# Kernel optimization log

Measured on AMD Instinct MI355X. Metric: run time of the kernel, lower is better.

Reference implementation:

```python
import jax, jax.numpy as jnp
import numpy as np

N_NODES = 100000
N_EDGES = 3200000
IN_CH = 256
HIDDEN = 64
OUT_CH = 128


def setup_inputs() -> dict:
    key = jax.random.key(0)
    ks = jax.random.split(key, 6)
    x = jax.random.normal(ks[0], (N_NODES, IN_CH), dtype=jnp.float32)
    edge_index = jax.random.randint(ks[1], (2, N_EDGES), 0, N_NODES, dtype=jnp.int64)
    W1 = jax.random.normal(ks[2], (IN_CH, HIDDEN), dtype=jnp.float32) * (1.0 / np.sqrt(IN_CH))
    b1 = jnp.zeros((HIDDEN,), dtype=jnp.float32)
    W2 = jax.random.normal(ks[3], (HIDDEN, OUT_CH), dtype=jnp.float32) * (1.0 / np.sqrt(HIDDEN))
    b2 = jnp.zeros((OUT_CH,), dtype=jnp.float32)
    fcW = jax.random.normal(ks[4], (2, OUT_CH), dtype=jnp.float32) * (1.0 / np.sqrt(OUT_CH))
    fcb = jnp.zeros((2,), dtype=jnp.float32)
    return {"x": x, "edge_index": edge_index, "W1": W1, "b1": b1,
            "W2": W2, "b2": b2, "fcW": fcW, "fcb": fcb}


def _gcn_conv(x, edge_index, W, b):
    """PyG GCNConv: linear transform, add self-loops, symmetric D^-1/2 A D^-1/2 aggregation, bias."""
    N = x.shape[0]
    h = x @ W  # [N, F_out]
    loops = jnp.arange(N, dtype=edge_index.dtype)
    row = jnp.concatenate([edge_index[0], loops])  # source nodes
    col = jnp.concatenate([edge_index[1], loops])  # destination nodes
    deg = jax.ops.segment_sum(jnp.ones_like(col, dtype=h.dtype), col, num_segments=N)
    dinv = jnp.where(deg > 0, jax.lax.rsqrt(deg), 0.0)
    norm = dinv[row] * dinv[col]  # [E+N]
    out = jax.ops.segment_sum(h[row] * norm[:, None], col, num_segments=N)
    return out + b


def reference(x, edge_index, W1, b1, W2, b2, fcW, fcb):
    h = jax.nn.relu(_gcn_conv(x, edge_index, W1, b1))
    h = jax.nn.relu(_gcn_conv(h, edge_index, W2, b2))
    g = jnp.mean(h, axis=0)  # [OUT_CH]
    return g @ fcW.T + fcb   # [2]
```

## Files before the change

kernel.cpp:

```cpp
#include <hip/hip_runtime.h>

#define N_NODES 100000
#define N_EDGES 3200000
#define C_IN 256
#define C_H 64
#define C_OUT 128
#define NB 391
#define BCAP 16384
#define G2F 625
#define NTILES 6250
#define NT16 6250
#define G_GM 1563
#define CH1 8192

typedef unsigned int u32;
typedef unsigned short u16;
typedef unsigned char u8;
typedef unsigned long long u64;
typedef __attribute__((ext_vector_type(8))) short bf16x8;
typedef __attribute__((ext_vector_type(4))) float f32x4;

typedef __attribute__((address_space(3))) unsigned int l_u32;
typedef __attribute__((address_space(1))) const unsigned int g_u32;

__device__ __forceinline__ float bf2f(u16 u) {
    union { u32 i; float f; } v; v.i = ((u32)u) << 16; return v.f;
}
__device__ __forceinline__ u16 f2bf(float f) {
    union { float f; u32 i; } v; v.f = f;
    u32 x = v.i;
    return (u16)((x + 0x7fffu + ((x >> 16) & 1u)) >> 16);
}
__device__ __forceinline__ u8 f2fp8(float f) {
    union { float f; u32 i; } v; v.f = f;
    u32 s = (v.i >> 24) & 0x80u;
    float a = __builtin_fabsf(f);
    a = fminf(a, 448.f);
    if (a < 0.015625f) {
        int m = (int)__builtin_rintf(a * 512.f);
        return (u8)(s | (u32)m);
    }
    union { float ff; u32 i; } w; w.ff = a;
    u32 x = w.i;
    u32 r = x + 0x7FFFFu + ((x >> 20) & 1u);
    u32 E = (r >> 23) - 120u;
    u32 m = (r >> 20) & 7u;
    return (u8)(s | (E << 3) | m);
}

__device__ __forceinline__ void gll16(const void* gp, const void* lp) {
    __builtin_amdgcn_global_load_lds((g_u32*)gp, (l_u32*)lp, 16, 0, 0);
}

__global__ __launch_bounds__(256) void k_prep(const void* __restrict__ x, const void* __restrict__ ei,
                                              const void* __restrict__ W1, const void* __restrict__ W2,
                                              const void* __restrict__ b1, const void* __restrict__ b2,
                                              const void* __restrict__ fcW, const void* __restrict__ fcb,
                                              int* __restrict__ flags,
                                              u16* __restrict__ W1m, u16* __restrict__ W2m,
                                              u32* __restrict__ bucket_cnt,
                                              float* __restrict__ b1c, float* __restrict__ b2c,
                                              float* __restrict__ fcWc, float* __restrict__ fcbc) {
    __shared__ int sfb;
    int b = blockIdx.x, t = threadIdx.x;
    if (t < 64) {
        u32 wv = ((const u32*)x)[t];
        u32 low = wv & 0xffffu;
        int e = (int)((low >> 7) & 0xff);
        bool inw = (e > 96 && e < 160) || (low == 0);
        u64 m = __ballot(inw);
        if (t == 0) sfb = (__popcll(m) >= 60) ? 1 : 0;
    } else if (b == 0 && t < 128) {
        int i = t - 64;
        u32 wv = ((const u32*)ei)[2 * i + 1];
        u64 m = __ballot(wv == 0);
        if (i == 0) flags[1] = (m == ~0ull) ? 1 : 0;
    }
    __syncthreads();
    int isbf = sfb;
    if (b == 0 && t == 0) flags[0] = isbf;
    int i = b * 256 + t;
    if (i < NB) bucket_cnt[i] = 0;
    if (i < C_IN * C_H) {
        const u16* w1b = (const u16*)W1; const float* w1f = (const float*)W1;
        int j = i & 7, lane = (i >> 3) & 63, nt = (i >> 9) & 3, k0 = i >> 11;
        int k = k0 * 32 + ((lane >> 4) & 3) * 8 + j;
        int n = nt * 16 + (lane & 15);
        W1m[i] = isbf ? w1b[k * C_H + n] : f2bf(w1f[k * C_H + n]);
    } else {
        int i2 = i - C_IN * C_H;
        const u16* w2b = (const u16*)W2; const float* w2f = (const float*)W2;
        int j = i2 & 7, lane = (i2 >> 3) & 63, nt = (i2 >> 9) & 7, k0 = (i2 >> 12) & 1;
        int k = k0 * 32 + ((lane >> 4) & 3) * 8 + j;
        int n = nt * 16 + (lane & 15);
        W2m[i2] = isbf ? w2b[k * C_OUT + n] : f2bf(w2f[k * C_OUT + n]);
    }
    if (b == 0) {
        if (isbf) {
            const u16* p1 = (const u16*)b1;  const u16* p2 = (const u16*)b2;
            const u16* pw = (const u16*)fcW; const u16* pb = (const u16*)fcb;
            for (int q = t; q < C_H; q += 256) b1c[q] = bf2f(p1[q]);
            for (int q = t; q < C_OUT; q += 256) b2c[q] = bf2f(p2[q]);
            for (int q = t; q < 2 * C_OUT; q += 256) fcWc[q] = bf2f(pw[q]);
            for (int q = t; q < 2; q += 256) fcbc[q] = bf2f(pb[q]);
        } else {
            const float* p1 = (const float*)b1;  const float* p2 = (const float*)b2;
            const float* pw = (const float*)fcW; const float* pb = (const float*)fcb;
            for (int q = t; q < C_H; q += 256) b1c[q] = p1[q];
            for (int q = t; q < C_OUT; q += 256) b2c[q] = p2[q];
            for (int q = t; q < 2 * C_OUT; q += 256) fcWc[q] = pw[q];
            for (int q = t; q < 2; q += 256) fcbc[q] = pb[q];
        }
    }
}

__global__ __launch_bounds__(512) void k_scatter1(const int* __restrict__ ei,
                                                  const int* __restrict__ flags,
                                                  u32* __restrict__ bucket_cnt,
                                                  u32* __restrict__ ebuf) {
    __shared__ u32 cnt[NB];
    __shared__ u32 lcur[NB];
    __shared__ u32 gbase[NB];
    __shared__ u32 lofs[512];
    __shared__ u32 stp[CH1];
    __shared__ u16 stb[CH1];
    int t = threadIdx.x;
    int is64 = flags[1];
    int e0 = blockIdx.x * CH1;
    int nv = min(CH1, N_EDGES - e0);
    for (int i = t; i < NB; i += 512) { cnt[i] = 0; lcur[i] = 0; }
    __syncthreads();
    for (int i = t; i < nv; i += 512) {
        int e = e0 + i;
        int d = is64 ? ei[2 * (N_EDGES + e)] : ei[N_EDGES + e];
        atomicAdd(&cnt[d >> 8], 1u);
    }
    __syncthreads();
    u32 v = (t < NB) ? cnt[t] : 0;
    lofs[t] = v;
    __syncthreads();
    for (int off = 1; off < 512; off <<= 1) {
        u32 a = (t >= off) ? lofs[t - off] : 0;
        __syncthreads();
        lofs[t] += a;
        __syncthreads();
    }
    u32 excl = lofs[t] - v;
    __syncthreads();
    lofs[t] = excl;
    __syncthreads();
    for (int i = t; i < nv; i += 512) {
        int e = e0 + i;
        int d, s;
        if (is64) { d = ei[2 * (N_EDGES + e)]; s = ei[2 * e]; }
        else      { d = ei[N_EDGES + e];       s = ei[e]; }
        int b = d >> 8;
        u32 slot = lofs[b] + atomicAdd(&lcur[b], 1u);
        stp[slot] = ((u32)(d & 255) << 20) | (u32)s;
        stb[slot] = (u16)b;
    }
    __syncthreads();
    for (int b = t; b < NB; b += 512) {
        u32 c = cnt[b];
        gbase[b] = c ? atomicAdd(&bucket_cnt[b], c) : 0;
    }
    __syncthreads();
    for (int s = t; s < nv; s += 512) {
        int b = stb[s];
        ebuf[(size_t)b * BCAP + gbase[b] + (s - lofs[b])] = stp[s];
    }
}

__global__ __launch_bounds__(256) void k_scatter2(const u32* __restrict__ bucket_cnt,
                                                  const u32* __restrict__ ebuf,
                                                  int* __restrict__ rowptr,
                                                  float* __restrict__ dinv,
                                                  int* __restrict__ csr) {
    __shared__ u32 ssum[256];
    __shared__ u32 snev;
    __shared__ int cnt[256];
    __shared__ int pfx[256];
    __shared__ int lcur[256];
    int b = blockIdx.x, t = threadIdx.x;
    u32 a = 0;
    for (int i = t; i < NB; i += 256) {
        u32 cv = bucket_cnt[i];
        if (i < b) a += cv;
        if (i == b) snev = cv;
    }
    ssum[t] = a;
    __syncthreads();
    for (int off = 128; off >= 1; off >>= 1) {
        if (t < off) ssum[t] += ssum[t + off];
        __syncthreads();
    }
    int ebeg = (int)ssum[0];
    int ne = (int)snev;
    const u32* src = ebuf + (size_t)b * BCAP;
    int sbeg = ebeg + (b << 8);
    cnt[t] = 0;
    lcur[t] = 0;
    __syncthreads();
    for (int i = t; i < ne; i += 256)
        atomicAdd(&cnt[(src[i] >> 20) & 255], 1);
    __syncthreads();
    int v = cnt[t];
    pfx[t] = v;
    __syncthreads();
    for (int off = 1; off < 256; off <<= 1) {
        int pv = (t >= off) ? pfx[t - off] : 0;
        __syncthreads();
        pfx[t] += pv;
        __syncthreads();
    }
    int node = (b << 8) + t;
    int rstart = sbeg + (pfx[t] - v) + t;
    if (node < N_NODES) {
        rowptr[node] = rstart;
        dinv[node] = rsqrtf((float)(v + 1));
        csr[rstart] = node << 6;
        if (node == N_NODES - 1) {
            rowptr[N_NODES] = rstart + v + 1;
            for (int i = 0; i < 64; ++i) csr[rstart + v + 1 + i] = 0;
        }
    }
    __syncthreads();
    for (int i = t; i < ne; i += 256) {
        u32 p = src[i];
        int dl = (p >> 20) & 255;
        int pos = sbeg + (pfx[dl] - cnt[dl]) + dl + 1 + atomicAdd(&lcur[dl], 1);
        csr[pos] = (int)((p & 0x1FFFFu) << 6);
    }
}

__global__ __launch_bounds__(256) void k_gemm1(const void* __restrict__ xv,
                                               const u16* __restrict__ W1m,
                                               const float* __restrict__ dinv,
                                               u8* __restrict__ g1,
                                               const int* __restrict__ flags) {
    __shared__ u16 wlds[C_IN * C_H];
    int t = threadIdx.x;
    int isbf = flags[0];
    {
        const uint4* src = (const uint4*)W1m;
        uint4* dst = (uint4*)wlds;
#pragma unroll
        for (int it = 0; it < 8; ++it) dst[t + it * 256] = src[t + it * 256];
    }
    __syncthreads();
    int w = t >> 6, lane = t & 63;
    int quad = lane >> 4, mrow = lane & 15;
    int m0 = blockIdx.x * 128 + w * 32;
    if (m0 >= N_NODES) return;

    bf16x8 a[2][8];
    if (isbf) {
        const u16* xb = (const u16*)xv;
#pragma unroll
        for (int mt = 0; mt < 2; ++mt)
#pragma unroll
            for (int k0 = 0; k0 < 8; ++k0)
                a[mt][k0] = *(const bf16x8*)(xb + (size_t)(m0 + mt * 16 + mrow) * C_IN + k0 * 32 + quad * 8);
    } else {
        const float* xf = (const float*)xv;
#pragma unroll
        for (int mt = 0; mt < 2; ++mt)
#pragma unroll
            for (int k0 = 0; k0 < 8; ++k0) {
                const float* p = xf + (size_t)(m0 + mt * 16 + mrow) * C_IN + k0 * 32 + quad * 8;
                float4 v0 = *(const float4*)p;
                float4 v1 = *(const float4*)(p + 4);
                bf16x8 r;
                r[0] = (short)f2bf(v0.x); r[1] = (short)f2bf(v0.y);
                r[2] = (short)f2bf(v0.z); r[3] = (short)f2bf(v0.w);
                r[4] = (short)f2bf(v1.x); r[5] = (short)f2bf(v1.y);
                r[6] = (short)f2bf(v1.z); r[7] = (short)f2bf(v1.w);
                a[mt][k0] = r;
            }
    }

    float dv0[4], dv1[4];
#pragma unroll
    for (int r = 0; r < 4; ++r) {
        dv0[r] = dinv[m0 + quad * 4 + r] * 16.f;
        dv1[r] = dinv[m0 + 16 + quad * 4 + r] * 16.f;
    }

#pragma unroll
    for (int nt = 0; nt < 4; ++nt) {
        bf16x8 b[8];
#pragma unroll
        for (int k0 = 0; k0 < 8; ++k0)
            b[k0] = *(const bf16x8*)&wlds[((k0 * 4 + nt) * 64 + lane) * 8];
        f32x4 acc0 = {0.f, 0.f, 0.f, 0.f};
        f32x4 acc1 = {0.f, 0.f, 0.f, 0.f};
#pragma unroll
        for (int k0 = 0; k0 < 8; ++k0) {
            acc0 = __builtin_amdgcn_mfma_f32_16x16x32_bf16(a[0][k0], b[k0], acc0, 0, 0, 0);
            acc1 = __builtin_amdgcn_mfma_f32_16x16x32_bf16(a[1][k0], b[k0], acc1, 0, 0, 0);
        }
        int ch = nt * 16 + mrow;
#pragma unroll
        for (int r = 0; r < 4; ++r) {
            g1[(size_t)(m0 + quad * 4 + r) * C_H + ch] = f2fp8(acc0[r] * dv0[r]);
            g1[(size_t)(m0 + 16 + quad * 4 + r) * C_H + ch] = f2fp8(acc1[r] * dv1[r]);
        }
    }
}

template <int MODE>
__global__ __launch_bounds__(256) void k_gatherM(const int* __restrict__ rowptr,
                                                 const int* __restrict__ csrb,
                                                 const float* __restrict__ dinv,
                                                 const u8* __restrict__ gt,
                                                 const float* __restrict__ bias,
                                                 void* __restrict__ out) {
    __shared__ __align__(16) u8 hsb[4][4096];
    __shared__ u64 lut8[81];
    int t = threadIdx.x;
    if (t < 81) {
        int s = t / 9, e = t - s * 9;
        u32 lo = 0, hi = 0;
#pragma unroll
        for (int j = 0; j < 4; ++j) if (j >= s && j < e) lo |= 0x18u << (8 * j);
#pragma unroll
        for (int j = 4; j < 8; ++j) if (j >= s && j < e) hi |= 0x18u << (8 * (j - 4));
        lut8[t] = ((u64)hi << 32) | lo;
    }
    __syncthreads();
    int w = t >> 6, lane = t & 63;
    int tile = blockIdx.x * 4 + w;
    if (tile >= NT16) return;

    int g16 = lane >> 4, c = lane & 15;
    int n0 = tile << 4;
    int lo = rowptr[n0 + c];
    int hi = rowptr[n0 + c + 1];
    int beg = __shfl(lo, 0, 64);
    int end = __shfl(hi, 15, 64);
    int ridx = lane >> 2;
    int bq = (lane & 3) * 16;
    const char* gb = (const char*)gt;
    u8* hw = hsb[w];
    f32x4 acc0 = {0.f, 0.f, 0.f, 0.f}, acc1 = acc0, acc2 = acc0, acc3 = acc0;
    int nch = (end - beg + 31) >> 5;
    int cb = beg;
    {
        u32 o0 = (u32)csrb[cb + ridx];
        u32 o1 = (u32)csrb[cb + 16 + ridx];
        gll16(gb + o0 + bq, hw);
        gll16(gb + o1 + bq, hw + 1024);
        asm volatile("" ::: "memory");
    }
    for (int ci = 0; ci < nch; ++ci) {
        int cbn = cb + 32;
        bool more = (ci + 1 < nch);
        u32 n0o = 0, n1o = 0;
        if (more) {
            n0o = (u32)csrb[cbn + ridx];
            n1o = (u32)csrb[cbn + 16 + ridx];
        }
        if (more) asm volatile("s_waitcnt vmcnt(2)" ::: "memory");
        else      asm volatile("s_waitcnt vmcnt(0)" ::: "memory");
        const u8* lp = hw + ((ci & 1) << 11) + g16 * 512 + c;
        int cbg = cb + g16 * 8;
        int s0 = min(max(lo - cbg, 0), 8);
        int e0 = min(max(hi - cbg, 0), 8);
        union P8 { u32 u[2]; long l; } pa, pb0, pb1, pb2, pb3;
        u64 av = lut8[s0 * 9 + e0];
        pa.u[0] = (u32)av; pa.u[1] = (u32)(av >> 32);
#define LDB(P, O)                                                                           \
        P.u[0] = (u32)lp[O] | ((u32)lp[O + 64] << 8) | ((u32)lp[O + 128] << 16) |           \
                 ((u32)lp[O + 192] << 24);                                                  \
        P.u[1] = (u32)lp[O + 256] | ((u32)lp[O + 320] << 8) | ((u32)lp[O + 384] << 16) |    \
                 ((u32)lp[O + 448] << 24);
        LDB(pb0, 0) LDB(pb1, 16) LDB(pb2, 32) LDB(pb3, 48)
#undef LDB
        acc0 = __builtin_amdgcn_mfma_f32_16x16x32_fp8_fp8(pa.l, pb0.l, acc0, 0, 0, 0);
        acc1 = __builtin_amdgcn_mfma_f32_16x16x32_fp8_fp8(pa.l, pb1.l, acc1, 0, 0, 0);
        acc2 = __builtin_amdgcn_mfma_f32_16x16x32_fp8_fp8(pa.l, pb2.l, acc2, 0, 0, 0);
        acc3 = __builtin_amdgcn_mfma_f32_16x16x32_fp8_fp8(pa.l, pb3.l, acc3, 0, 0, 0);
        if (more) {
            int bo = ((ci + 1) & 1) << 11;
            gll16(gb + n0o + bq, hw + bo);
            gll16(gb + n1o + bq, hw + bo + 1024);
            asm volatile("" ::: "memory");
        }
        cb = cbn;
    }
    float dv[4];
    int nb = n0 + g16 * 4;
#pragma unroll
    for (int r = 0; r < 4; ++r) dv[r] = dinv[nb + r];
    if (MODE == 0) {
        u8* ob = (u8*)out + (size_t)nb * C_H + c;
#define EPI(ACC, CHT)                                                                       \
        {                                                                                   \
            float bs = bias[CHT * 16 + c];                                                  \
            _Pragma("unroll")                                                               \
            for (int r = 0; r < 4; ++r)                                                     \
                ob[r * C_H + CHT * 16] =                                                    \
                    f2fp8(16.f * dv[r] * fmaxf(dv[r] * ACC[r] + bs, 0.f));                  \
        }
        EPI(acc0, 0) EPI(acc1, 1) EPI(acc2, 2) EPI(acc3, 3)
#undef EPI
    } else {
        u16* ob = (u16*)out + (size_t)nb * C_H + c;
#define EPI(ACC, CHT)                                                                       \
        {                                                                                   \
            _Pragma("unroll")                                                               \
            for (int r = 0; r < 4; ++r)                                                     \
                ob[r * C_H + CHT * 16] = f2bf(dv[r] * ACC[r]);                              \
        }
        EPI(acc0, 0) EPI(acc1, 1) EPI(acc2, 2) EPI(acc3, 3)
#undef EPI
    }
}

__global__ __launch_bounds__(256) void k_fused2(const u16* __restrict__ aggb,
                                                const u16* __restrict__ W2m,
                                                const float* __restrict__ b2c,
                                                float* __restrict__ partial) {
    __shared__ float psum[4 * 8 * 64];
    int t = threadIdx.x;
    int w = t >> 6, lane = t & 63;
    int quad = lane >> 4, m = lane & 15;

    bf16x8 b[2][8];
#pragma unroll
    for (int k0 = 0; k0 < 2; ++k0)
#pragma unroll
        for (int nt = 0; nt < 8; ++nt)
            b[k0][nt] = *(const bf16x8*)&W2m[((k0 * 8 + nt) * 64 + lane) * 8];

    float pacc[8] = {0.f, 0.f, 0.f, 0.f, 0.f, 0.f, 0.f, 0.f};
    float bias[8];
#pragma unroll
    for (int nt = 0; nt < 8; ++nt) bias[nt] = b2c[nt * 16 + m];

    for (int tile = blockIdx.x * 4 + w; tile < NTILES; tile += G2F * 4) {
        const u16* arow = aggb + (size_t)(tile * 16 + m) * C_H + quad * 8;
        bf16x8 a0 = *(const bf16x8*)(arow);
        bf16x8 a1 = *(const bf16x8*)(arow + 32);
#pragma unroll
        for (int nt = 0; nt < 8; ++nt) {
            f32x4 acc = {0.f, 0.f, 0.f, 0.f};
            acc = __builtin_amdgcn_mfma_f32_16x16x32_bf16(a0, b[0][nt], acc, 0, 0, 0);
            acc = __builtin_amdgcn_mfma_f32_16x16x32_bf16(a1, b[1][nt], acc, 0, 0, 0);
#pragma unroll
            for (int r = 0; r < 4; ++r)
                pacc[nt] += fmaxf(acc[r] + bias[nt], 0.f);
        }
    }
#pragma unroll
    for (int nt = 0; nt < 8; ++nt) psum[(w * 8 + nt) * 64 + lane] = pacc[nt];
    __syncthreads();
    if (t < 128) {
        int nt = t >> 4, m2 = t & 15;
        float s = 0.f;
#pragma unroll
        for (int ww = 0; ww < 4; ++ww)
#pragma unroll
            for (int q = 0; q < 4; ++q)
                s += psum[(ww * 8 + nt) * 64 + q * 16 + m2];
        partial[blockIdx.x * C_OUT + t] = s;
    }
}

__global__ __launch_bounds__(512) void k_final(const float* __restrict__ partial,
                                               const float* __restrict__ fcWc,
                                               const float* __restrict__ fcbc,
                                               void* __restrict__ out,
                                               const int* __restrict__ flags) {
    __shared__ float sm[512];
    __shared__ float red[256];
    int t = threadIdx.x;
    int f = t & 127, c = t >> 7;
    float s = 0.f;
    for (int b = c; b < G2F; b += 4) s += partial[b * 128 + f];
    sm[t] = s;
    __syncthreads();
    if (t < 128) {
        float gm = (sm[t] + sm[t + 128] + sm[t + 256] + sm[t + 384]) * (1.0f / (float)N_NODES);
        red[t] = gm * fcWc[t];
        red[128 + t] = gm * fcWc[128 + t];
    }
    __syncthreads();
    for (int off = 64; off >= 1; off >>= 1) {
        if (t < off) {
            red[t] += red[t + off];
            red[128 + t] += red[128 + t + off];
        }
        __syncthreads();
    }
    if (t == 0) {
        float o0 = red[0] + fcbc[0];
        float o1 = red[128] + fcbc[1];
        if (flags[0]) {
            u16* ob = (u16*)out;
            ob[0] = f2bf(o0);
            ob[1] = f2bf(o1);
        } else {
            float* of = (float*)out;
            of[0] = o0;
            of[1] = o1;
        }
    }
}

#define OFF_FLAGS   0u
#define OFF_DINV    512u
#define OFF_ROWPTR  400896u
#define OFF_BCNT    801280u
#define OFF_CSR     1201664u
#define OFF_H1      14402560u
#define OFF_A1      27202560u
#define OFF_AGG     40002560u
#define OFF_PART    52802560u
#define OFF_W1C     53122560u
#define OFF_W2C     53155328u
#define OFF_B1C     53171712u
#define OFF_B2C     53171968u
#define OFF_FCWC    53172480u
#define OFF_FCBC    53173504u
#define OFF_EBUF    53174272u

extern "C" void kernel_launch(void* const* d_in, const int* in_sizes, int n_in,
                              void* d_out, int out_size, void* d_ws, size_t ws_size,
                              hipStream_t stream) {
    (void)in_sizes; (void)n_in; (void)out_size; (void)ws_size;
    const void* x   = d_in[0];
    const int*  ei  = (const int*)d_in[1];
    const void* W1  = d_in[2];
    const void* b1  = d_in[3];
    const void* W2  = d_in[4];
    const void* b2  = d_in[5];
    const void* fcW = d_in[6];
    const void* fcb = d_in[7];

    char* ws = (char*)d_ws;
    int*   flags  = (int*)(ws + OFF_FLAGS);
    float* dinv   = (float*)(ws + OFF_DINV);
    int*   rowptr = (int*)(ws + OFF_ROWPTR);
    u32*   bcnt   = (u32*)(ws + OFF_BCNT);
    int*   csr    = (int*)(ws + OFF_CSR);
    u8*    g1     = (u8*)(ws + OFF_H1);
    u8*    a1s    = (u8*)(ws + OFF_A1);
    u16*   aggb   = (u16*)(ws + OFF_AGG);
    u32*   ebuf   = (u32*)(ws + OFF_EBUF);
    float* partial= (float*)(ws + OFF_PART);
    u16*   W1m    = (u16*)(ws + OFF_W1C);
    u16*   W2m    = (u16*)(ws + OFF_W2C);
    float* b1c    = (float*)(ws + OFF_B1C);
    float* b2c    = (float*)(ws + OFF_B2C);
    float* fcWc   = (float*)(ws + OFF_FCWC);
    float* fcbc   = (float*)(ws + OFF_FCBC);

    k_prep<<<96, 256, 0, stream>>>(x, ei, W1, W2, b1, b2, fcW, fcb,
                                   flags, W1m, W2m, bcnt, b1c, b2c, fcWc, fcbc);
    k_scatter1<<<NB, 512, 0, stream>>>(ei, flags, bcnt, ebuf);
    k_scatter2<<<NB, 256, 0, stream>>>(bcnt, ebuf, rowptr, dinv, csr);
    k_gemm1<<<(N_NODES + 127) / 128, 256, 0, stream>>>(x, W1m, dinv, g1, flags);
    k_gatherM<0><<<G_GM, 256, 0, stream>>>(rowptr, csr, dinv, g1, b1c, (void*)a1s);
    k_gatherM<1><<<G_GM, 256, 0, stream>>>(rowptr, csr, dinv, a1s, b2c, (void*)aggb);
    k_fused2<<<G2F, 256, 0, stream>>>(aggb, W2m, b2c, partial);
    k_final<<<1, 512, 0, stream>>>(partial, fcWc, fcbc, (void*)d_out, flags);
}
```

Before: 361.3 us.

## Interleave fp8 feature layout to replace byte LDS reads with dword loads and transpose

```diff
diff --git a/kernel.cpp b/kernel.cpp
--- a/kernel.cpp
+++ b/kernel.cpp
@@ -51,6 +51,18 @@
 __device__ __forceinline__ void gll16(const void* gp, const void* lp) {
     __builtin_amdgcn_global_load_lds((g_u32*)gp, (l_u32*)lp, 16, 0, 0);
 }
+
+#define BT4(a0, a1, a2, a3, r0, r1, r2, r3)                          \
+    {                                                                \
+        u32 t0 = (a0 & 0x00ff00ffu) | ((a1 & 0x00ff00ffu) << 8);     \
+        u32 t1 = ((a0 >> 8) & 0x00ff00ffu) | (a1 & 0xff00ff00u);     \
+        u32 t2 = (a2 & 0x00ff00ffu) | ((a3 & 0x00ff00ffu) << 8);     \
+        u32 t3 = ((a2 >> 8) & 0x00ff00ffu) | (a3 & 0xff00ff00u);     \
+        r0 = (t0 & 0xffffu) | (t2 << 16);                            \
+        r2 = (t0 >> 16) | (t2 & 0xffff0000u);                        \
+        r1 = (t1 & 0xffffu) | (t3 << 16);                            \
+        r3 = (t1 >> 16) | (t3 & 0xffff0000u);                        \
+    }
 
 __global__ __launch_bounds__(256) void k_prep(const void* __restrict__ x, const void* __restrict__ ei,
                                               const void* __restrict__ W1, const void* __restrict__ W2,
@@ -299,11 +311,11 @@
             acc0 = __builtin_amdgcn_mfma_f32_16x16x32_bf16(a[0][k0], b[k0], acc0, 0, 0, 0);
             acc1 = __builtin_amdgcn_mfma_f32_16x16x32_bf16(a[1][k0], b[k0], acc1, 0, 0, 0);
         }
-        int ch = nt * 16 + mrow;
+        int pos = mrow * 4 + nt;
 #pragma unroll
         for (int r = 0; r < 4; ++r) {
-            g1[(size_t)(m0 + quad * 4 + r) * C_H + ch] = f2fp8(acc0[r] * dv0[r]);
-            g1[(size_t)(m0 + 16 + quad * 4 + r) * C_H + ch] = f2fp8(acc1[r] * dv1[r]);
+            g1[(size_t)(m0 + quad * 4 + r) * C_H + pos] = f2fp8(acc0[r] * dv0[r]);
+            g1[(size_t)(m0 + 16 + quad * 4 + r) * C_H + pos] = f2fp8(acc1[r] * dv1[r]);
         }
     }
 }
@@ -332,75 +344,79 @@
     int tile = blockIdx.x * 4 + w;
     if (tile >= NT16) return;
 
-    int g16 = lane >> 4, c = lane & 15;
+    int cg = lane >> 4, c = lane & 15;
     int n0 = tile << 4;
     int lo = rowptr[n0 + c];
     int hi = rowptr[n0 + c + 1];
     int beg = __shfl(lo, 0, 64);
     int end = __shfl(hi, 15, 64);
-    int ridx = lane >> 2;
-    int bq = (lane & 3) * 16;
+    int rowA = ((lane >> 2) & 3) * 8 + (lane >> 4);
+    int rowB = rowA + 4;
+    int s16 = (lane & 3) * 16;
     const char* gb = (const char*)gt;
     u8* hw = hsb[w];
+    int bi = cg * 16 + c;
     f32x4 acc0 = {0.f, 0.f, 0.f, 0.f}, acc1 = acc0, acc2 = acc0, acc3 = acc0;
     int nch = (end - beg + 31) >> 5;
     int cb = beg;
     {
-        u32 o0 = (u32)csrb[cb + ridx];
-        u32 o1 = (u32)csrb[cb + 16 + ridx];
-        gll16(gb + o0 + bq, hw);
-        gll16(gb + o1 + bq, hw + 1024);
+        u32 oA = (u32)csrb[cb + rowA];
+        u32 oB = (u32)csrb[cb + rowB];
+        gll16(gb + oA + s16, hw);
+        gll16(gb + oB + s16, hw + 1024);
         asm volatile("" ::: "memory");
     }
     for (int ci = 0; ci < nch; ++ci) {
         int cbn = cb + 32;
         bool more = (ci + 1 < nch);
-        u32 n0o = 0, n1o = 0;
+        u32 nA = 0, nB = 0;
         if (more) {
-            n0o = (u32)csrb[cbn + ridx];
-            n1o = (u32)csrb[cbn + 16 + ridx];
+            nA = (u32)csrb[cbn + rowA];
+            nB = (u32)csrb[cbn + rowB];
         }
         if (more) asm volatile("s_waitcnt vmcnt(2)" ::: "memory");
         else      asm volatile("s_waitcnt vmcnt(0)" ::: "memory");
-        const u8* lp = hw + ((ci & 1) << 11) + g16 * 512 + c;
-        int cbg = cb + g16 * 8;
+        const u32* hb = (const u32*)(hw + ((ci & 1) << 11));
+        u32 w0 = hb[bi], w1 = hb[bi + 64], w2 = hb[bi + 128], w3 = hb[bi + 192];
+        u32 w4 = hb[bi + 256], w5 = hb[bi + 320], w6 = hb[bi + 384], w7 = hb[bi + 448];
+        u32 l0, l1, l2, l3, h0, h1, h2, h3;
+        BT4(w0, w1, w2, w3, l0, l1, l2, l3)
+        BT4(w4, w5, w6, w7, h0, h1, h2, h3)
+        int cbg = cb + cg * 8;
         int s0 = min(max(lo - cbg, 0), 8);
         int e0 = min(max(hi - cbg, 0), 8);
         union P8 { u32 u[2]; long l; } pa, pb0, pb1, pb2, pb3;
         u64 av = lut8[s0 * 9 + e0];
         pa.u[0] = (u32)av; pa.u[1] = (u32)(av >> 32);
-#define LDB(P, O)                                                                           \
-        P.u[0] = (u32)lp[O] | ((u32)lp[O + 64] << 8) | ((u32)lp[O + 128] << 16) |           \
-                 ((u32)lp[O + 192] << 24);                                                  \
-        P.u[1] = (u32)lp[O + 256] | ((u32)lp[O + 320] << 8) | ((u32)lp[O + 384] << 16) |    \
-                 ((u32)lp[O + 448] << 24);
-        LDB(pb0, 0) LDB(pb1, 16) LDB(pb2, 32) LDB(pb3, 48)
-#undef LDB
+        pb0.u[0] = l0; pb0.u[1] = h0;
+        pb1.u[0] = l1; pb1.u[1] = h1;
+        pb2.u[0] = l2; pb2.u[1] = h2;
+        pb3.u[0] = l3; pb3.u[1] = h3;
         acc0 = __builtin_amdgcn_mfma_f32_16x16x32_fp8_fp8(pa.l, pb0.l, acc0, 0, 0, 0);
         acc1 = __builtin_amdgcn_mfma_f32_16x16x32_fp8_fp8(pa.l, pb1.l, acc1, 0, 0, 0);
         acc2 = __builtin_amdgcn_mfma_f32_16x16x32_fp8_fp8(pa.l, pb2.l, acc2, 0, 0, 0);
         acc3 = __builtin_amdgcn_mfma_f32_16x16x32_fp8_fp8(pa.l, pb3.l, acc3, 0, 0, 0);
         if (more) {
             int bo = ((ci + 1) & 1) << 11;
-            gll16(gb + n0o + bq, hw + bo);
-            gll16(gb + n1o + bq, hw + bo + 1024);
+            gll16(gb + nA + s16, hw + bo);
+            gll16(gb + nB + s16, hw + bo + 1024);
             asm volatile("" ::: "memory");
         }
         cb = cbn;
     }
     float dv[4];
-    int nb = n0 + g16 * 4;
-#pragma unroll
-    for (int r = 0; r < 4; ++r) dv[r] = dinv[nb + r];
+    int nb = n0 + cg * 4;
+#pragma unroll
+    for (int q = 0; q < 4; ++q) dv[q] = dinv[nb + q];
     if (MODE == 0) {
-        u8* ob = (u8*)out + (size_t)nb * C_H + c;
+        u8* ob = (u8*)out + (size_t)nb * C_H + c * 4;
 #define EPI(ACC, CHT)                                                                       \
         {                                                                                   \
             float bs = bias[CHT * 16 + c];                                                  \
             _Pragma("unroll")                                                               \
-            for (int r = 0; r < 4; ++r)                                                     \
-                ob[r * C_H + CHT * 16] =                                                    \
-                    f2fp8(16.f * dv[r] * fmaxf(dv[r] * ACC[r] + bs, 0.f));                  \
+            for (int q = 0; q < 4; ++q)                                                     \
+                ob[q * C_H + CHT] =                                                         \
+                    f2fp8(16.f * dv[q] * fmaxf(dv[q] * ACC[q] + bs, 0.f));                  \
         }
         EPI(acc0, 0) EPI(acc1, 1) EPI(acc2, 2) EPI(acc3, 3)
 #undef EPI
@@ -409,8 +425,8 @@
 #define EPI(ACC, CHT)                                                                       \
         {                                                                                   \
             _Pragma("unroll")                                                               \
-            for (int r = 0; r < 4; ++r)                                                     \
-                ob[r * C_H + CHT * 16] = f2bf(dv[r] * ACC[r]);                              \
+            for (int q = 0; q < 4; ++q)                                                     \
+                ob[q * C_H + CHT * 16] = f2bf(dv[q] * ACC[q]);                              \
         }
         EPI(acc0, 0) EPI(acc1, 1) EPI(acc2, 2) EPI(acc3, 3)
 #undef EPI
```

Measured after the change: 357.7 us. About the same (-1.0%).
